# Optimization experiments

Measured on AMD Instinct MI355X. Metric: run time of the kernel, lower is better.

## Reference

```python
import jax, jax.numpy as jnp
import numpy as np

D_MODEL = 512
HEADS = 8
FF_HIDDEN = 1024
EPS = 1e-6


def setup_inputs() -> dict:
    key = jax.random.key(0)
    ks = jax.random.split(key, 12)
    s = 1.0 / np.sqrt(D_MODEL)
    inp = {
        'x': jax.random.normal(ks[0], (2, 4096, D_MODEL), dtype=jnp.float32),
        'Wq': jax.random.normal(ks[1], (D_MODEL, D_MODEL), dtype=jnp.float32) * s,
        'bq': jnp.zeros((D_MODEL,), jnp.float32),
        'Wk': jax.random.normal(ks[2], (D_MODEL, D_MODEL), dtype=jnp.float32) * s,
        'bk': jnp.zeros((D_MODEL,), jnp.float32),
        'Wv': jax.random.normal(ks[3], (D_MODEL, D_MODEL), dtype=jnp.float32) * s,
        'bv': jnp.zeros((D_MODEL,), jnp.float32),
        'Wo': jax.random.normal(ks[4], (D_MODEL, D_MODEL), dtype=jnp.float32) * s,
        'bo': jnp.zeros((D_MODEL,), jnp.float32),
        'a1': jnp.ones((D_MODEL,), jnp.float32),
        'b1': jnp.zeros((D_MODEL,), jnp.float32),
        'a2': jnp.ones((D_MODEL,), jnp.float32),
        'b2': jnp.zeros((D_MODEL,), jnp.float32),
        'W1': jax.random.normal(ks[5], (D_MODEL, FF_HIDDEN), dtype=jnp.float32) * s,
        'c1': jnp.zeros((FF_HIDDEN,), jnp.float32),
        'W2': jax.random.normal(ks[6], (FF_HIDDEN, D_MODEL), dtype=jnp.float32) * (1.0 / np.sqrt(FF_HIDDEN)),
        'c2': jnp.zeros((D_MODEL,), jnp.float32),
    }
    return inp


def _layer_norm(x, a, b):
    # Faithful to source: uses unbiased std (torch default) and divides by (std + eps)
    mean = jnp.mean(x, axis=-1, keepdims=True)
    std = jnp.std(x, axis=-1, keepdims=True, ddof=1)
    return a * ((x - mean) / (std + EPS)) + b


def _encoder_block(x, Wq, bq, Wk, bk, Wv, bv, Wo, bo, a1, b1, a2, b2, W1, c1, W2, c2):
    B, S, D = x.shape
    H, dk = HEADS, D // HEADS
    q = (x @ Wq + bq).reshape(B, S, H, dk).transpose(0, 2, 1, 3)  # [B,H,S,dk]
    k = (x @ Wk + bk).reshape(B, S, H, dk).transpose(0, 2, 1, 3)
    v = (x @ Wv + bv).reshape(B, S, H, dk).transpose(0, 2, 1, 3)
    scores = jnp.einsum('bhqd,bhkd->bhqk', q, k) / np.sqrt(dk)
    probs = jax.nn.softmax(scores, axis=-1)
    attn = jnp.einsum('bhqk,bhkd->bhqd', probs, v)
    concat = attn.transpose(0, 2, 1, 3).reshape(B, S, D)
    attn_out = concat @ Wo + bo
    x = _layer_norm(x + attn_out, a1, b1)  # dropout = identity (eval mode)
    ffn = jax.nn.relu(x @ W1 + c1) @ W2 + c2
    return _layer_norm(x + ffn, a2, b2)


def reference(x, Wq, bq, Wk, bk, Wv, bv, Wo, bo, a1, b1, a2, b2, W1, c1, W2, c2):
    return _encoder_block(x, Wq, bq, Wk, bk, Wv, bv, Wo, bo, a1, b1, a2, b2, W1, c1, W2, c2)
```

## Files before the change

### kernel.cpp

```cpp
#include <hip/hip_runtime.h>
#include <stdint.h>

typedef short short8 __attribute__((ext_vector_type(8)));
typedef short short4v __attribute__((ext_vector_type(4)));
typedef float f32x4 __attribute__((ext_vector_type(4)));
typedef float f32x16 __attribute__((ext_vector_type(16)));
typedef unsigned int u32x4 __attribute__((ext_vector_type(4)));

#define LOG2E 1.44269504088896f
#define QSCALE (0.125f * LOG2E)

__device__ __forceinline__ unsigned short f2b(float f) {
  union { float f; unsigned int u; } x; x.f = f;
  unsigned int u = x.u;
  unsigned int r = (u + 0x7fffu + ((u >> 16) & 1u)) >> 16;
  return (unsigned short)r;
}
__device__ __forceinline__ float b2f(unsigned short s) {
  union { unsigned int u; float f; } x; x.u = ((unsigned int)s) << 16;
  return x.f;
}
__device__ __forceinline__ void gl16(const void* g, void* l) {
  __builtin_amdgcn_global_load_lds((const __attribute__((address_space(1))) void*)g,
                                   (__attribute__((address_space(3))) void*)l, 16, 0, 0);
}
__device__ __forceinline__ unsigned int cvtpk(float lo, float hi) {
  unsigned int r;
  asm("v_cvt_pk_bf16_f32 %0, %1, %2" : "=v"(r) : "v"(lo), "v"(hi));
  return r;
}
__device__ __forceinline__ void plswap(unsigned int& a, unsigned int& b) {
  asm volatile("v_permlane32_swap_b32 %0, %1" : "+v"(a), "+v"(b));
}

__global__ __launch_bounds__(256) void prep_k(
    const float* __restrict__ X, unsigned short* __restrict__ Xb,
    const float* __restrict__ Wq, const float* __restrict__ Wk,
    const float* __restrict__ Wv, const float* __restrict__ Wo,
    const float* __restrict__ W1, const float* __restrict__ W2,
    unsigned short* __restrict__ WqkvT, unsigned short* __restrict__ WoT,
    unsigned short* __restrict__ W1T, unsigned short* __restrict__ W2T,
    const float* __restrict__ bq, const float* __restrict__ bk,
    const float* __restrict__ bv, float* __restrict__ Bqkv) {
  __shared__ float t[64][65];
  int bid = blockIdx.x, tid = threadIdx.x;
  if (bid < 2048) {
    int i = bid * 256 + tid;
    const float* p = X + (size_t)i * 8;
    float4 a = *(const float4*)(p);
    float4 b = *(const float4*)(p + 4);
    short8 o;
    o[0] = (short)f2b(a.x); o[1] = (short)f2b(a.y);
    o[2] = (short)f2b(a.z); o[3] = (short)f2b(a.w);
    o[4] = (short)f2b(b.x); o[5] = (short)f2b(b.y);
    o[6] = (short)f2b(b.z); o[7] = (short)f2b(b.w);
    *(short8*)(Xb + (size_t)i * 8) = o;
    return;
  }
  if (bid == 2560) {
    for (int i = tid; i < 1536; i += 256) {
      float v = (i < 512) ? bq[i] * QSCALE : (i < 1024 ? bk[i - 512] : bv[i - 1024]);
      Bqkv[i] = v;
    }
    return;
  }
  int idx = bid - 2048;
  const float* W; unsigned short* WT; int K, N, kb, nb; float scale = 1.0f;
  if (idx < 256) {
    int sec = idx >> 6, local = idx & 63;
    K = 512; N = 512; kb = local >> 3; nb = local & 7;
    if (sec == 0) { W = Wq; WT = WqkvT; scale = QSCALE; }
    else if (sec == 1) { W = Wk; WT = WqkvT + 512 * 512; }
    else if (sec == 2) { W = Wv; WT = WqkvT + 2 * 512 * 512; }
    else { W = Wo; WT = WoT; }
  } else if (idx < 384) {
    int local = idx - 256; K = 512; N = 1024; kb = local >> 4; nb = local & 15;
    W = W1; WT = W1T;
  } else {
    int local = idx - 384; K = 1024; N = 512; kb = local >> 3; nb = local & 7;
    W = W2; WT = W2T;
  }
  int k0 = kb * 64, n0 = nb * 64;
  for (int i = tid; i < 4096; i += 256) {
    int r = i >> 6, c = i & 63;
    t[r][c] = W[(size_t)(k0 + r) * N + n0 + c];
  }
  __syncthreads();
  for (int i = tid; i < 4096; i += 256) {
    int r = i >> 6, c = i & 63;
    WT[(size_t)(n0 + r) * K + k0 + c] = f2b(t[c][r] * scale);
  }
}

template <int EPI>
__global__ __launch_bounds__(256) void gemm_bt(
    const unsigned short* __restrict__ A, const unsigned short* __restrict__ BT,
    const float* __restrict__ bias, float* __restrict__ Cf,
    unsigned short* __restrict__ Cb, int M, int N, int K) {
  __shared__ unsigned short As[128 * 32];
  __shared__ unsigned short Bs[128 * 32];
  int t = threadIdx.x, w = t >> 6, l = t & 63;
  int bm = blockIdx.x, bn = blockIdx.y;
  int wm = w >> 1, wn = w & 1;
  int g = l >> 4, ln = l & 15;
  f32x4 acc[4][4] = {};
  const unsigned short* Arow = A + (size_t)bm * 128 * K;
  const unsigned short* Brow = BT + (size_t)bn * 128 * K;
  int nk = K >> 5;
  for (int kt = 0; kt < nk; ++kt) {
    int k0 = kt * 32;
#pragma unroll
    for (int i = 0; i < 2; ++i) {
      int cl = i * 256 + t;
      int r = cl >> 2, c = cl & 3;
      char* ldsA = (char*)As + (size_t)(i * 256 + w * 64) * 16;
      char* ldsB = (char*)Bs + (size_t)(i * 256 + w * 64) * 16;
      gl16(Arow + (size_t)r * K + k0 + c * 8, ldsA);
      gl16(Brow + (size_t)r * K + k0 + c * 8, ldsB);
    }
    __syncthreads();
    short8 af[4], bf[4];
    int ko = g * 8;
#pragma unroll
    for (int i = 0; i < 4; ++i)
      af[i] = *(const short8*)&As[(wm * 64 + i * 16 + ln) * 32 + ko];
#pragma unroll
    for (int j = 0; j < 4; ++j)
      bf[j] = *(const short8*)&Bs[(wn * 64 + j * 16 + ln) * 32 + ko];
    __builtin_amdgcn_s_setprio(1);
#pragma unroll
    for (int i = 0; i < 4; ++i)
#pragma unroll
      for (int j = 0; j < 4; ++j)
        acc[i][j] = __builtin_amdgcn_mfma_f32_16x16x32_bf16(af[i], bf[j], acc[i][j], 0, 0, 0);
    __builtin_amdgcn_s_setprio(0);
    __syncthreads();
  }
#pragma unroll
  for (int i = 0; i < 4; ++i) {
    int row = bm * 128 + wm * 64 + i * 16 + g * 4;
#pragma unroll
    for (int j = 0; j < 4; ++j) {
      int col = bn * 128 + wn * 64 + j * 16 + ln;
      float bv = bias[col];
      float vv[4];
#pragma unroll
      for (int r = 0; r < 4; ++r) {
        float v = acc[i][j][r] + bv;
        if constexpr (EPI == 2) v = v > 0.f ? v : 0.f;
        vv[r] = v;
      }
      if constexpr (EPI == 3) {
        if (col < 1024) {
#pragma unroll
          for (int r = 0; r < 4; ++r)
            Cb[(size_t)(col >> 9) * 4194304 + (size_t)(row + r) * 512 + (col & 511)] = f2b(vv[r]);
        } else {
          short4v pk;
#pragma unroll
          for (int r = 0; r < 4; ++r) pk[r] = (short)f2b(vv[r]);
          *(short4v*)((unsigned short*)Cf +
                      (size_t)((row >> 12) * 512 + (col & 511)) * 4096 + (row & 4095)) = pk;
        }
      } else {
#pragma unroll
        for (int r = 0; r < 4; ++r)
          Cb[(size_t)(row + r) * N + col] = f2b(vv[r]);
      }
    }
  }
}

template <bool WB>
__global__ __launch_bounds__(512) void gemmln_k(
    const unsigned short* __restrict__ A, const unsigned short* __restrict__ BT,
    const float* __restrict__ bias, const float* __restrict__ X,
    const float* __restrict__ gamma, const float* __restrict__ beta,
    float* __restrict__ outf, unsigned short* __restrict__ outb, int K) {
  __shared__ unsigned short As[32 * 32];
  __shared__ unsigned short Bs[512 * 32];
  __shared__ float stats[8][32][2];
  __shared__ float minv[32][2];
  int tid = threadIdx.x, wv = tid >> 6, lane = tid & 63;
  int g = lane >> 4, ln = lane & 15;
  int bm = blockIdx.x;
  f32x4 acc[2][4] = {};
  const unsigned short* Arow = A + (size_t)bm * 32 * K;
  int nk = K >> 5;
  for (int kt = 0; kt < nk; ++kt) {
    int k0 = kt * 32;
    if (tid < 128) {
      int r = tid >> 2, c = tid & 3;
      gl16(Arow + (size_t)r * K + k0 + c * 8, (char*)As + tid * 16);
    }
#pragma unroll
    for (int i = 0; i < 4; ++i) {
      int u = i * 512 + tid;
      int r = u >> 2, c = u & 3;
      gl16(BT + (size_t)r * K + k0 + c * 8, (char*)Bs + (size_t)u * 16);
    }
    __syncthreads();
    short8 af[2], bf[4];
#pragma unroll
    for (int i = 0; i < 2; ++i)
      af[i] = *(const short8*)&As[(i * 16 + ln) * 32 + g * 8];
#pragma unroll
    for (int j = 0; j < 4; ++j)
      bf[j] = *(const short8*)&Bs[(wv * 64 + j * 16 + ln) * 32 + g * 8];
    __builtin_amdgcn_s_setprio(1);
#pragma unroll
    for (int i = 0; i < 2; ++i)
#pragma unroll
      for (int j = 0; j < 4; ++j)
        acc[i][j] = __builtin_amdgcn_mfma_f32_16x16x32_bf16(af[i], bf[j], acc[i][j], 0, 0, 0);
    __builtin_amdgcn_s_setprio(0);
    __syncthreads();
  }
  int row0 = bm * 32;
  float v[2][4][4];
  float ps[8], pss[8];
#pragma unroll
  for (int k = 0; k < 8; ++k) { ps[k] = 0.f; pss[k] = 0.f; }
#pragma unroll
  for (int i = 0; i < 2; ++i)
#pragma unroll
    for (int j = 0; j < 4; ++j) {
      int col = wv * 64 + j * 16 + ln;
      float bv = bias[col];
#pragma unroll
      for (int r = 0; r < 4; ++r) {
        int row = i * 16 + g * 4 + r;
        float t = acc[i][j][r] + bv + X[(size_t)(row0 + row) * 512 + col];
        v[i][j][r] = t;
        ps[i * 4 + r] += t; pss[i * 4 + r] += t * t;
      }
    }
#pragma unroll
  for (int off = 1; off < 16; off <<= 1) {
#pragma unroll
    for (int k = 0; k < 8; ++k) {
      ps[k] += __shfl_xor(ps[k], off);
      pss[k] += __shfl_xor(pss[k], off);
    }
  }
  if (ln == 0) {
#pragma unroll
    for (int i = 0; i < 2; ++i)
#pragma unroll
      for (int r = 0; r < 4; ++r) {
        stats[wv][i * 16 + g * 4 + r][0] = ps[i * 4 + r];
        stats[wv][i * 16 + g * 4 + r][1] = pss[i * 4 + r];
      }
  }
  __syncthreads();
  if (tid < 32) {
    float S = 0.f, SS = 0.f;
#pragma unroll
    for (int w2 = 0; w2 < 8; ++w2) { S += stats[w2][tid][0]; SS += stats[w2][tid][1]; }
    float mean = S * (1.f / 512.f);
    float var = fmaxf((SS - 512.f * mean * mean) * (1.f / 511.f), 0.f);
    minv[tid][0] = mean;
    minv[tid][1] = 1.f / (sqrtf(var) + 1e-6f);
  }
  __syncthreads();
#pragma unroll
  for (int i = 0; i < 2; ++i)
#pragma unroll
    for (int j = 0; j < 4; ++j) {
      int col = wv * 64 + j * 16 + ln;
      float gm = gamma[col], bt2 = beta[col];
#pragma unroll
      for (int r = 0; r < 4; ++r) {
        int row = i * 16 + g * 4 + r;
        float o = gm * ((v[i][j][r] - minv[row][0]) * minv[row][1]) + bt2;
        outf[(size_t)(row0 + row) * 512 + col] = o;
        if constexpr (WB) outb[(size_t)(row0 + row) * 512 + col] = f2b(o);
      }
    }
}

__global__ __launch_bounds__(256, 2) void attn_k(
    const unsigned short* __restrict__ Q, const unsigned short* __restrict__ Kb,
    const unsigned short* __restrict__ Vt, unsigned short* __restrict__ Opart,
    float* __restrict__ L) {
  __shared__ unsigned short Ks[2][4096];
  __shared__ unsigned short Vs[3][4096];
  int tid = threadIdx.x, wv = tid >> 6, lane = tid & 63;
  int l31 = lane & 31, hi = lane >> 5;
  int qb = blockIdx.x, bh = blockIdx.y, z = blockIdx.z;
  int b = bh >> 3, h = bh & 7;
  int q0 = qb * 256 + wv * 64;
  int kvbase = z * 2048;

  short8 qfA[4], qfB[4];
  {
    const unsigned short* qpA = Q + (size_t)(b * 4096 + q0 + l31) * 512 + h * 64;
    const unsigned short* qpB = qpA + 32 * 512;
#pragma unroll
    for (int ks = 0; ks < 4; ++ks) {
      qfA[ks] = *(const short8*)(qpA + ks * 16 + hi * 8);
      qfB[ks] = *(const short8*)(qpB + ks * 16 + hi * 8);
    }
  }

  short8 ones;
#pragma unroll
  for (int j = 0; j < 8; ++j) ones[j] = (short)0x3F80;

  const f32x16 Z = {};
  f32x16 oA0 = {}, oA1 = {}, oB0 = {}, oB1 = {}, laccA = {}, laccB = {};

  int skk[2], sc[2];
#pragma unroll
  for (int i = 0; i < 2; ++i) {
    int u = i * 256 + tid;
    int r2 = u >> 4, s = u & 15;
    skk[i] = 2 * r2 + (s & 1);
    sc[i] = ((s >> 1) ^ (r2 & 7)) * 8;
  }

  auto stage = [&](char* kb_lds, char* vb_lds, int kv) {
    const unsigned short* ksrc = Kb + (size_t)(b * 4096 + kv) * 512 + h * 64;
    const unsigned short* vsrc = Vt + (size_t)(bh * 64) * 4096 + kv;
#pragma unroll
    for (int i = 0; i < 2; ++i) {
      gl16(ksrc + (size_t)skk[i] * 512 + sc[i], kb_lds + (size_t)(i * 256 + wv * 64) * 16);
      gl16(vsrc + (size_t)skk[i] * 4096 + sc[i], vb_lds + (size_t)(i * 256 + wv * 64) * 16);
    }
  };

  int r2a = l31 >> 1, par = l31 & 1, perm = r2a & 7;
  int rdb = r2a * 256 + (par << 4);

  auto qk = [&](const char* kbase, f32x16& sA0, f32x16& sA1, f32x16& sB0, f32x16& sB1) {
    __builtin_amdgcn_s_setprio(1);
#pragma unroll
    for (int ks = 0; ks < 4; ++ks) {
      int c16 = ks * 2 + hi;
      int byteA = rdb + (((c16 ^ perm) << 1) << 4);
      short8 k0 = *(const short8*)(kbase + byteA);
      short8 k1 = *(const short8*)(kbase + byteA + 4096);
      if (ks == 0) {
        sA0 = __builtin_amdgcn_mfma_f32_32x32x16_bf16(k0, qfA[0], Z, 0, 0, 0);
        sA1 = __builtin_amdgcn_mfma_f32_32x32x16_bf16(k1, qfA[0], Z, 0, 0, 0);
        sB0 = __builtin_amdgcn_mfma_f32_32x32x16_bf16(k0, qfB[0], Z, 0, 0, 0);
        sB1 = __builtin_amdgcn_mfma_f32_32x32x16_bf16(k1, qfB[0], Z, 0, 0, 0);
      } else {
        sA0 = __builtin_amdgcn_mfma_f32_32x32x16_bf16(k0, qfA[ks], sA0, 0, 0, 0);
        sA1 = __builtin_amdgcn_mfma_f32_32x32x16_bf16(k1, qfA[ks], sA1, 0, 0, 0);
        sB0 = __builtin_amdgcn_mfma_f32_32x32x16_bf16(k0, qfB[ks], sB0, 0, 0, 0);
        sB1 = __builtin_amdgcn_mfma_f32_32x32x16_bf16(k1, qfB[ks], sB1, 0, 0, 0);
      }
    }
    __builtin_amdgcn_s_setprio(0);
  };

  auto pv = [&](const char* vbase, const short8* pfA, const short8* pfB) {
    __builtin_amdgcn_s_setprio(1);
#pragma unroll
    for (int ks = 0; ks < 4; ++ks) {
      int c16 = ks * 2 + hi;
      int byteA = rdb + (((c16 ^ perm) << 1) << 4);
      short8 v0 = *(const short8*)(vbase + byteA);
      short8 v1 = *(const short8*)(vbase + byteA + 4096);
      oA0 = __builtin_amdgcn_mfma_f32_32x32x16_bf16(v0, pfA[ks], oA0, 0, 0, 0);
      oA1 = __builtin_amdgcn_mfma_f32_32x32x16_bf16(v1, pfA[ks], oA1, 0, 0, 0);
      oB0 = __builtin_amdgcn_mfma_f32_32x32x16_bf16(v0, pfB[ks], oB0, 0, 0, 0);
      oB1 = __builtin_amdgcn_mfma_f32_32x32x16_bf16(v1, pfB[ks], oB1, 0, 0, 0);
      laccA = __builtin_amdgcn_mfma_f32_32x32x16_bf16(ones, pfA[ks], laccA, 0, 0, 0);
      laccB = __builtin_amdgcn_mfma_f32_32x32x16_bf16(ones, pfB[ks], laccB, 0, 0, 0);
    }
    __builtin_amdgcn_s_setprio(0);
  };

  auto exppack = [&](f32x16& s0, f32x16& s1, short8* pf) {
#pragma unroll
    for (int r = 0; r < 16; ++r) s0[r] = __builtin_amdgcn_exp2f(s0[r]);
#pragma unroll
    for (int r = 0; r < 16; ++r) s1[r] = __builtin_amdgcn_exp2f(s1[r]);
    unsigned int u0 = cvtpk(s0[0], s0[1]), u1 = cvtpk(s0[4], s0[5]);
    plswap(u0, u1);
    unsigned int u2 = cvtpk(s0[2], s0[3]), u3 = cvtpk(s0[6], s0[7]);
    plswap(u2, u3);
    unsigned int u4 = cvtpk(s0[8], s0[9]), u5 = cvtpk(s0[12], s0[13]);
    plswap(u4, u5);
    unsigned int u6 = cvtpk(s0[10], s0[11]), u7 = cvtpk(s0[14], s0[15]);
    plswap(u6, u7);
    union { u32x4 u; short8 s; } cv;
    cv.u = (u32x4){u0, u2, u1, u3}; pf[0] = cv.s;
    cv.u = (u32x4){u4, u6, u5, u7}; pf[1] = cv.s;
    unsigned int w0 = cvtpk(s1[0], s1[1]), w1 = cvtpk(s1[4], s1[5]);
    plswap(w0, w1);
    unsigned int w2 = cvtpk(s1[2], s1[3]), w3 = cvtpk(s1[6], s1[7]);
    plswap(w2, w3);
    unsigned int w4 = cvtpk(s1[8], s1[9]), w5 = cvtpk(s1[12], s1[13]);
    plswap(w4, w5);
    unsigned int w6 = cvtpk(s1[10], s1[11]), w7 = cvtpk(s1[14], s1[15]);
    plswap(w6, w7);
    cv.u = (u32x4){w0, w2, w1, w3}; pf[2] = cv.s;
    cv.u = (u32x4){w4, w6, w5, w7}; pf[3] = cv.s;
  };

  char* k0b = (char*)&Ks[0][0];
  char* k1b = (char*)&Ks[1][0];
  char* vA = (char*)&Vs[0][0];
  char* vB = (char*)&Vs[1][0];
  char* vC = (char*)&Vs[2][0];
  stage(k0b, vA, kvbase);
  __syncthreads();
  stage(k1b, vB, kvbase + 64);

  f32x16 sA0, sA1, sB0, sB1;
  qk(k0b, sA0, sA1, sB0, sB1);
  short8 pfA[4], pfB[4];
  exppack(sA0, sA1, pfA);
  exppack(sB0, sB1, pfB);

#pragma unroll 1
  for (int t = 1; t < 32; ++t) {
    __syncthreads();
    char* kr = (t & 1) ? k1b : k0b;
    char* kw = (t & 1) ? k0b : k1b;
    if (t < 31) stage(kw, vC, kvbase + (t + 1) * 64);
    qk(kr, sA0, sA1, sB0, sB1);
    pv(vA, pfA, pfB);
    exppack(sA0, sA1, pfA);
    exppack(sB0, sB1, pfB);
    char* tmp = vA; vA = vB; vB = vC; vC = tmp;
  }
  pv(vA, pfA, pfB);

  int plane = z * 16 + bh;
  unsigned short* op = Opart + (size_t)plane * 262144;
  int qA = q0 + l31, qB = q0 + 32 + l31;
#pragma unroll
  for (int r = 0; r < 16; ++r) {
    int dr = (r & 3) + 8 * (r >> 2) + 4 * hi;
    op[(size_t)dr * 4096 + qA] = f2b(oA0[r]);
    op[(size_t)(dr + 32) * 4096 + qA] = f2b(oA1[r]);
    op[(size_t)dr * 4096 + qB] = f2b(oB0[r]);
    op[(size_t)(dr + 32) * 4096 + qB] = f2b(oB1[r]);
  }
  if (hi == 0) {
    L[(size_t)plane * 4096 + qA] = laccA[0];
    L[(size_t)plane * 4096 + qB] = laccB[0];
  }
}

__global__ __launch_bounds__(256) void comb_k(const unsigned short* __restrict__ Opart,
                                              const float* __restrict__ L,
                                              unsigned short* __restrict__ O) {
  __shared__ float sli[64];
  __shared__ unsigned short tt[64][80];
  int tid = threadIdx.x;
  int qt = blockIdx.x, bh = blockIdx.y;
  int b = bh >> 3, h = bh & 7;
  int q0 = qt * 64;
  if (tid < 64) {
    int q = q0 + tid;
    sli[tid] = 1.0f / (L[(size_t)bh * 4096 + q] + L[(size_t)(16 + bh) * 4096 + q]);
  }
  __syncthreads();
  const unsigned short* p0 = Opart + (size_t)bh * 262144;
  const unsigned short* p1 = Opart + (size_t)(16 + bh) * 262144;
  int d = tid >> 2, qg = tid & 3;
#pragma unroll
  for (int i = 0; i < 16; ++i) {
    int qq = qg * 16 + i;
    size_t idx = (size_t)d * 4096 + q0 + qq;
    tt[qq][d] = f2b((b2f(p0[idx]) + b2f(p1[idx])) * sli[qq]);
  }
  __syncthreads();
  int qr = tid >> 2, dc = tid & 3;
  short8 v0 = *(const short8*)&tt[qr][dc * 16];
  short8 v1 = *(const short8*)&tt[qr][dc * 16 + 8];
  size_t row = (size_t)(b * 4096 + q0 + qr);
  *(short8*)(O + row * 512 + h * 64 + dc * 16) = v0;
  *(short8*)(O + row * 512 + h * 64 + dc * 16 + 8) = v1;
}

extern "C" void kernel_launch(void* const* d_in, const int* in_sizes, int n_in,
                              void* d_out, int out_size, void* d_ws, size_t ws_size,
                              hipStream_t stream) {
  const float* x  = (const float*)d_in[0];
  const float* Wq = (const float*)d_in[1];
  const float* bq = (const float*)d_in[2];
  const float* Wk = (const float*)d_in[3];
  const float* bk = (const float*)d_in[4];
  const float* Wv = (const float*)d_in[5];
  const float* bv = (const float*)d_in[6];
  const float* Wo = (const float*)d_in[7];
  const float* bo = (const float*)d_in[8];
  const float* a1 = (const float*)d_in[9];
  const float* b1 = (const float*)d_in[10];
  const float* a2 = (const float*)d_in[11];
  const float* b2 = (const float*)d_in[12];
  const float* W1 = (const float*)d_in[13];
  const float* c1 = (const float*)d_in[14];
  const float* W2 = (const float*)d_in[15];
  const float* c2 = (const float*)d_in[16];

  char* ws = (char*)d_ws;
  const size_t MB = 1024 * 1024;
  unsigned short* Xb  = (unsigned short*)(ws + 0);
  unsigned short* Qb  = (unsigned short*)(ws + 8 * MB);
  unsigned short* Kbf = (unsigned short*)(ws + 16 * MB);
  float* L = (float*)(ws + 24 * MB);
  unsigned short* Vtb = (unsigned short*)(ws + 32 * MB);
  unsigned short* WqkvT = (unsigned short*)(ws + 40 * MB);
  unsigned short* WoT = (unsigned short*)(ws + 41 * MB + 512 * 1024);
  unsigned short* W1T = (unsigned short*)(ws + 42 * MB);
  unsigned short* W2T = (unsigned short*)(ws + 43 * MB);
  unsigned short* Opart = (unsigned short*)(ws + 44 * MB);
  float* Bqkv = (float*)(ws + 44 * MB);
  float* Y1 = (float*)(ws + 60 * MB);
  unsigned short* Att = Xb;
  unsigned short* Y1b = Qb;
  unsigned short* Hb  = Kbf;

  prep_k<<<2561, 256, 0, stream>>>(x, Xb, Wq, Wk, Wv, Wo, W1, W2,
                                   WqkvT, WoT, W1T, W2T, bq, bk, bv, Bqkv);

  gemm_bt<3><<<dim3(64, 12), 256, 0, stream>>>(Xb, WqkvT, Bqkv, (float*)Vtb, Qb, 8192, 1536, 512);

  attn_k<<<dim3(16, 16, 2), 256, 0, stream>>>(Qb, Kbf, Vtb, Opart, L);
  comb_k<<<dim3(64, 16), 256, 0, stream>>>(Opart, L, Att);

  gemmln_k<true><<<256, 512, 0, stream>>>(Att, WoT, bo, x, a1, b1, Y1, Y1b, 512);
  gemm_bt<2><<<dim3(64, 8), 256, 0, stream>>>(Y1b, W1T, c1, nullptr, Hb, 8192, 1024, 512);
  gemmln_k<false><<<256, 512, 0, stream>>>(Hb, W2T, c2, Y1, a2, b2, (float*)d_out, nullptr, 1024);
}
```

Measured before the change: 194.8 us.

## Fuse split-KV attention combine into output-projection GEMM+LayerNorm kernel

Removes the separate comb_k kernel. The Wo GEMM+LN kernel now reads the two partial attention outputs and their L sums directly, normalises them, and stores the full 32x512 bf16 A tile in LDS once before the K loop. This saves one kernel launch and one global write and read of the attention output. In exchange, each block does a prologue with strided global reads (Opart is [d][q]), scalar LDS writes with possible bank conflicts, and holds a larger LDS footprint, which may lower occupancy.

```diff
diff --git a/kernel.cpp b/kernel.cpp
--- a/kernel.cpp
+++ b/kernel.cpp
@@ -171,27 +171,63 @@
   }
 }
 
-template <bool WB>
+template <int AMODE, bool WB>
 __global__ __launch_bounds__(512) void gemmln_k(
     const unsigned short* __restrict__ A, const unsigned short* __restrict__ BT,
     const float* __restrict__ bias, const float* __restrict__ X,
     const float* __restrict__ gamma, const float* __restrict__ beta,
-    float* __restrict__ outf, unsigned short* __restrict__ outb, int K) {
-  __shared__ unsigned short As[32 * 32];
+    float* __restrict__ outf, unsigned short* __restrict__ outb,
+    const unsigned short* __restrict__ Opart, const float* __restrict__ L,
+    int K) {
+  __shared__ unsigned short As[AMODE ? 32 * 520 : 32 * 32];
   __shared__ unsigned short Bs[512 * 32];
   __shared__ float stats[8][32][2];
   __shared__ float minv[32][2];
+  __shared__ float sli[8][32];
   int tid = threadIdx.x, wv = tid >> 6, lane = tid & 63;
   int g = lane >> 4, ln = lane & 15;
   int bm = blockIdx.x;
+  int row0 = bm * 32;
   f32x4 acc[2][4] = {};
-  const unsigned short* Arow = A + (size_t)bm * 32 * K;
+
+  if constexpr (AMODE == 1) {
+    int b = row0 >> 12;
+    int q0 = row0 & 4095;
+    if (tid < 256) {
+      int h = tid >> 5, qq = tid & 31;
+      int bh = b * 8 + h;
+      float s = L[(size_t)bh * 4096 + q0 + qq] + L[(size_t)(16 + bh) * 4096 + q0 + qq];
+      sli[h][qq] = 1.0f / s;
+    }
+    __syncthreads();
+    int col = tid;
+    int h = col >> 6, d = col & 63;
+    int bh = b * 8 + h;
+    const unsigned short* p0 = Opart + (size_t)bh * 262144 + (size_t)d * 4096 + q0;
+    const unsigned short* p1 = Opart + (size_t)(16 + bh) * 262144 + (size_t)d * 4096 + q0;
+#pragma unroll
+    for (int i = 0; i < 4; ++i) {
+      short8 a = *(const short8*)(p0 + i * 8);
+      short8 c = *(const short8*)(p1 + i * 8);
+#pragma unroll
+      for (int j = 0; j < 8; ++j) {
+        int qq = i * 8 + j;
+        float s = (b2f((unsigned short)a[j]) + b2f((unsigned short)c[j])) * sli[h][qq];
+        As[qq * 520 + col] = f2b(s);
+      }
+    }
+    __syncthreads();
+  }
+
+  const unsigned short* Arow = (AMODE == 0) ? (A + (size_t)bm * 32 * K) : nullptr;
   int nk = K >> 5;
   for (int kt = 0; kt < nk; ++kt) {
     int k0 = kt * 32;
-    if (tid < 128) {
-      int r = tid >> 2, c = tid & 3;
-      gl16(Arow + (size_t)r * K + k0 + c * 8, (char*)As + tid * 16);
+    if constexpr (AMODE == 0) {
+      if (tid < 128) {
+        int r = tid >> 2, c = tid & 3;
+        gl16(Arow + (size_t)r * K + k0 + c * 8, (char*)As + tid * 16);
+      }
     }
 #pragma unroll
     for (int i = 0; i < 4; ++i) {
@@ -202,8 +238,12 @@
     __syncthreads();
     short8 af[2], bf[4];
 #pragma unroll
-    for (int i = 0; i < 2; ++i)
-      af[i] = *(const short8*)&As[(i * 16 + ln) * 32 + g * 8];
+    for (int i = 0; i < 2; ++i) {
+      if constexpr (AMODE == 1)
+        af[i] = *(const short8*)&As[(i * 16 + ln) * 520 + k0 + g * 8];
+      else
+        af[i] = *(const short8*)&As[(i * 16 + ln) * 32 + g * 8];
+    }
 #pragma unroll
     for (int j = 0; j < 4; ++j)
       bf[j] = *(const short8*)&Bs[(wv * 64 + j * 16 + ln) * 32 + g * 8];
@@ -216,7 +256,6 @@
     __builtin_amdgcn_s_setprio(0);
     __syncthreads();
   }
-  int row0 = bm * 32;
   float v[2][4][4];
   float ps[8], pss[8];
 #pragma unroll
@@ -447,38 +486,6 @@
   }
 }
 
-__global__ __launch_bounds__(256) void comb_k(const unsigned short* __restrict__ Opart,
-                                              const float* __restrict__ L,
-                                              unsigned short* __restrict__ O) {
-  __shared__ float sli[64];
-  __shared__ unsigned short tt[64][80];
-  int tid = threadIdx.x;
-  int qt = blockIdx.x, bh = blockIdx.y;
-  int b = bh >> 3, h = bh & 7;
-  int q0 = qt * 64;
-  if (tid < 64) {
-    int q = q0 + tid;
-    sli[tid] = 1.0f / (L[(size_t)bh * 4096 + q] + L[(size_t)(16 + bh) * 4096 + q]);
-  }
-  __syncthreads();
-  const unsigned short* p0 = Opart + (size_t)bh * 262144;
-  const unsigned short* p1 = Opart + (size_t)(16 + bh) * 262144;
-  int d = tid >> 2, qg = tid & 3;
-#pragma unroll
-  for (int i = 0; i < 16; ++i) {
-    int qq = qg * 16 + i;
-    size_t idx = (size_t)d * 4096 + q0 + qq;
-    tt[qq][d] = f2b((b2f(p0[idx]) + b2f(p1[idx])) * sli[qq]);
-  }
-  __syncthreads();
-  int qr = tid >> 2, dc = tid & 3;
-  short8 v0 = *(const short8*)&tt[qr][dc * 16];
-  short8 v1 = *(const short8*)&tt[qr][dc * 16 + 8];
-  size_t row = (size_t)(b * 4096 + q0 + qr);
-  *(short8*)(O + row * 512 + h * 64 + dc * 16) = v0;
-  *(short8*)(O + row * 512 + h * 64 + dc * 16 + 8) = v1;
-}
-
 extern "C" void kernel_launch(void* const* d_in, const int* in_sizes, int n_in,
                               void* d_out, int out_size, void* d_ws, size_t ws_size,
                               hipStream_t stream) {
@@ -514,7 +521,6 @@
   unsigned short* Opart = (unsigned short*)(ws + 44 * MB);
   float* Bqkv = (float*)(ws + 44 * MB);
   float* Y1 = (float*)(ws + 60 * MB);
-  unsigned short* Att = Xb;
   unsigned short* Y1b = Qb;
   unsigned short* Hb  = Kbf;
 
@@ -524,9 +530,10 @@
   gemm_bt<3><<<dim3(64, 12), 256, 0, stream>>>(Xb, WqkvT, Bqkv, (float*)Vtb, Qb, 8192, 1536, 512);
 
   attn_k<<<dim3(16, 16, 2), 256, 0, stream>>>(Qb, Kbf, Vtb, Opart, L);
-  comb_k<<<dim3(64, 16), 256, 0, stream>>>(Opart, L, Att);
-
-  gemmln_k<true><<<256, 512, 0, stream>>>(Att, WoT, bo, x, a1, b1, Y1, Y1b, 512);
+
+  gemmln_k<1, true><<<256, 512, 0, stream>>>(nullptr, WoT, bo, x, a1, b1, Y1, Y1b,
+                                             Opart, L, 512);
   gemm_bt<2><<<dim3(64, 8), 256, 0, stream>>>(Y1b, W1T, c1, nullptr, Hb, 8192, 1024, 512);
-  gemmln_k<false><<<256, 512, 0, stream>>>(Hb, W2T, c2, Y1, a2, b2, (float*)d_out, nullptr, 1024);
-}
+  gemmln_k<0, false><<<256, 512, 0, stream>>>(Hb, W2T, c2, Y1, a2, b2, (float*)d_out, nullptr,
+                                              nullptr, nullptr, 1024);
+}
```

Result: no change. 192.9 us (-1.0%).
